# Kernel optimization log

Measured on AMD Instinct MI355X. Metric: run time of the kernel, lower is better.

## Reference

```python
import jax, jax.numpy as jnp
import numpy as np

N_NODES = 100000


def gcn_conv(x, W, b, src, dst, n_nodes):
    """PyG GCNConv: out = D^{-1/2} (A + I) D^{-1/2} X W + b."""
    h = x @ W  # [N, F_out]
    # add self-loops
    loop = jnp.arange(n_nodes, dtype=src.dtype)
    s = jnp.concatenate([src, loop])
    d = jnp.concatenate([dst, loop])
    # symmetric normalization (deg counts incoming edges incl. self-loop)
    deg = jax.ops.segment_sum(jnp.ones_like(d, dtype=h.dtype), d, num_segments=n_nodes)
    dinv = jnp.where(deg > 0, jax.lax.rsqrt(deg), 0.0)
    coef = dinv[s] * dinv[d]  # [E+N]
    msg = h[s] * coef[:, None]  # gather + scale
    out = jax.ops.segment_sum(msg, d, num_segments=n_nodes)  # scatter-add
    return out + b


def setup_inputs() -> dict:
    key = jax.random.key(0)
    k1, k2, k3, k4, k5, k6 = jax.random.split(key, 6)
    in_dim, hidden_dim, out_dim = 128, 64, 64
    n_edges = 1000000
    x = jax.random.normal(k1, (N_NODES, in_dim), dtype=jnp.float32)
    edge_index = jax.random.randint(k2, (2, n_edges), 0, N_NODES, dtype=jnp.int64)
    # glorot-style init for GCN weights
    W1 = jax.random.normal(k3, (in_dim, hidden_dim), dtype=jnp.float32) / np.sqrt(in_dim)
    b1 = jnp.zeros((hidden_dim,), dtype=jnp.float32)
    W2 = jax.random.normal(k4, (hidden_dim, out_dim), dtype=jnp.float32) / np.sqrt(hidden_dim)
    b2 = jnp.zeros((out_dim,), dtype=jnp.float32)
    return {"x": x, "edge_index": edge_index, "W1": W1, "b1": b1, "W2": W2, "b2": b2}


def reference(x, edge_index, W1, b1, W2, b2):
    src, dst = edge_index[0], edge_index[1]
    h = jax.nn.relu(gcn_conv(x, W1, b1, src, dst, N_NODES))
    out = gcn_conv(h, W2, b2, src, dst, N_NODES)
    return out
```

## Files before the change

kernel.cpp:

```cpp
#include <hip/hip_runtime.h>


#define MD 48

typedef __attribute__((ext_vector_type(8))) short bf16x8;
typedef __attribute__((ext_vector_type(4))) float f32x4;
typedef __attribute__((ext_vector_type(2))) float f32x2;
typedef __attribute__((ext_vector_type(4))) int   i32x4;
typedef __attribute__((ext_vector_type(4))) unsigned u32x4;

__device__ inline float bf2f(unsigned short v) {
    unsigned u = (unsigned)v << 16;
    return __builtin_bit_cast(float, u);
}
__device__ inline unsigned short f2bf(float f) {
    unsigned u = __builtin_bit_cast(unsigned, f);
    unsigned r = (u + 0x7FFFu + ((u >> 16) & 1u)) >> 16;
    return (unsigned short)r;
}

__device__ inline void convW_one(const float* __restrict__ W, short* __restrict__ Wth,
                                 short* __restrict__ Wtl, int K, int k, int f) {
    float v = W[k * 64 + f];
    unsigned b = __builtin_bit_cast(unsigned, v);
    unsigned hb = b & 0xFFFF0000u;
    float d = v - __builtin_bit_cast(float, hb);
    unsigned lb = __builtin_bit_cast(unsigned, d);
    Wth[f * K + k] = (short)(hb >> 16);
    Wtl[f * K + k] = (short)(lb >> 16);
}

__global__ __launch_bounds__(256) void k_prep(int* __restrict__ cnt, int n, int nbz,
                                              const float* __restrict__ W1,
                                              short* __restrict__ W1th, short* __restrict__ W1tl,
                                              const float* __restrict__ W2,
                                              short* __restrict__ W2th, short* __restrict__ W2tl) {
    const int b = blockIdx.x;
    if (b < nbz) {
        int i = b * 256 + threadIdx.x;
        if (i < n) cnt[i] = 0;
    } else if (b < nbz + 128) {
        if (threadIdx.x < 64) convW_one(W1, W1th, W1tl, 128, b - nbz, threadIdx.x);
    } else {
        if (threadIdx.x < 64) convW_one(W2, W2th, W2tl, 64, b - nbz - 128, threadIdx.x);
    }
}

__global__ __launch_bounds__(256) void k_fill_xcd(const int* __restrict__ src,
                                                  const int* __restrict__ dst, int E,
                                                  int* __restrict__ cnt,
                                                  int* __restrict__ col_ell,
                                                  int npx, int N) {
    const int myxcd = blockIdx.x & 7;
    const int lo = myxcd * npx;
    const int hi = lo + npx;
    const int vb = blockIdx.x >> 3;
    const int nvb = gridDim.x >> 3;
    const int tid = vb * 256 + threadIdx.x;
    const int nthr = nvb * 256;
    for (int base = tid * 4; base < E; base += nthr * 4) {
        i32x4 d4 = *(const i32x4*)&dst[base];
#pragma unroll
        for (int k = 0; k < 4; ++k) {
            int d = d4[k];
            if (d >= lo && d < hi) {
                int p = atomicAdd(&cnt[d], 1);
                if (p < MD) col_ell[(size_t)p * N + d] = src[base + k];
            }
        }
    }
}

template <int K>
__global__ __launch_bounds__(256) void k_mm_f32A(const float* __restrict__ X,
                                                 const short* __restrict__ Wth,
                                                 const short* __restrict__ Wtl,
                                                 const int* __restrict__ cnt,
                                                 unsigned short* __restrict__ G, int n) {
    const int lane = threadIdx.x & 63;
    const int w = threadIdx.x >> 6;
    const int r0 = lane & 15;
    const int kq = lane >> 4;
    const int arow = blockIdx.x * 64 + w * 16 + r0;
    const float* xrow = X + (size_t)(arow < n ? arow : n - 1) * K;

    f32x4 acc[4] = {};
#pragma unroll
    for (int kc = 0; kc < K / 32; ++kc) {
        const int ks = kc * 32 + kq * 8;
        float xv[8];
        *(f32x4*)&xv[0] = __builtin_nontemporal_load((const f32x4*)&xrow[ks]);
        *(f32x4*)&xv[4] = __builtin_nontemporal_load((const f32x4*)&xrow[ks + 4]);
        bf16x8 ah, al;
#pragma unroll
        for (int j = 0; j < 8; ++j) {
            unsigned b = __builtin_bit_cast(unsigned, xv[j]);
            unsigned hb = b & 0xFFFF0000u;
            float d = xv[j] - __builtin_bit_cast(float, hb);
            unsigned lb = __builtin_bit_cast(unsigned, d);
            ah[j] = (short)(hb >> 16);
            al[j] = (short)(lb >> 16);
        }
#pragma unroll
        for (int c = 0; c < 4; ++c) {
            bf16x8 bh = *(const bf16x8*)&Wth[(c * 16 + r0) * K + ks];
            bf16x8 bl = *(const bf16x8*)&Wtl[(c * 16 + r0) * K + ks];
            acc[c] = __builtin_amdgcn_mfma_f32_16x16x32_bf16(ah, bh, acc[c], 0, 0, 0);
            acc[c] = __builtin_amdgcn_mfma_f32_16x16x32_bf16(ah, bl, acc[c], 0, 0, 0);
            acc[c] = __builtin_amdgcn_mfma_f32_16x16x32_bf16(al, bh, acc[c], 0, 0, 0);
        }
    }
    const int orow = blockIdx.x * 64 + w * 16 + kq * 4;
#pragma unroll
    for (int rg = 0; rg < 4; ++rg) {
        int gr = orow + rg;
        if (gr < n) {
            float di = rsqrtf((float)(cnt[gr] + 1));
#pragma unroll
            for (int c = 0; c < 4; ++c)
                G[(size_t)gr * 64 + c * 16 + r0] = f2bf(acc[c][rg] * di);
        }
    }
}

__global__ __launch_bounds__(256) void k_mm_bf16A(const unsigned short* __restrict__ A,
                                                  const short* __restrict__ Wth,
                                                  const short* __restrict__ Wtl,
                                                  const int* __restrict__ cnt,
                                                  unsigned short* __restrict__ G, int n) {
    constexpr int K = 64;
    const int lane = threadIdx.x & 63;
    const int w = threadIdx.x >> 6;
    const int r0 = lane & 15;
    const int kq = lane >> 4;
    const int arow = blockIdx.x * 64 + w * 16 + r0;
    const unsigned short* ar = A + (size_t)(arow < n ? arow : n - 1) * K;

    f32x4 acc[4] = {};
#pragma unroll
    for (int kc = 0; kc < K / 32; ++kc) {
        const int ks = kc * 32 + kq * 8;
        bf16x8 a = __builtin_nontemporal_load((const bf16x8*)&ar[ks]);
#pragma unroll
        for (int c = 0; c < 4; ++c) {
            bf16x8 bh = *(const bf16x8*)&Wth[(c * 16 + r0) * K + ks];
            bf16x8 bl = *(const bf16x8*)&Wtl[(c * 16 + r0) * K + ks];
            acc[c] = __builtin_amdgcn_mfma_f32_16x16x32_bf16(a, bh, acc[c], 0, 0, 0);
            acc[c] = __builtin_amdgcn_mfma_f32_16x16x32_bf16(a, bl, acc[c], 0, 0, 0);
        }
    }
    const int orow = blockIdx.x * 64 + w * 16 + kq * 4;
#pragma unroll
    for (int rg = 0; rg < 4; ++rg) {
        int gr = orow + rg;
        if (gr < n) {
            float di = rsqrtf((float)(cnt[gr] + 1));
#pragma unroll
            for (int c = 0; c < 4; ++c)
                G[(size_t)gr * 64 + c * 16 + r0] = f2bf(acc[c][rg] * di);
        }
    }
}

template <bool RELU, bool OUTBF>
__global__ __launch_bounds__(256) void k_gather8(const unsigned short* __restrict__ g,
                                                 const int* __restrict__ cntArr,
                                                 const int* __restrict__ col_ell,
                                                 const float* __restrict__ bias,
                                                 void* __restrict__ dest, int n, int N) {
    const int node = blockIdx.x * 4 + (threadIdx.x >> 6);
    if (node >= n) return;
    const int lane = threadIdx.x & 63;
    const int grp = lane >> 3;
    const int fl = lane & 7;
    const int cn = cntArr[node];
    const int lc = min(cn, MD);
    const float dn = rsqrtf((float)(cn + 1));
    const int cl = min(lane, MD - 1);
    const int myidx = col_ell[(size_t)cl * N + node];

    f32x2 acc2[4] = {};
    if (grp == 0) {
        u32x4 u = *(const u32x4*)&g[(size_t)node * 64 + fl * 8];
#pragma unroll
        for (int k = 0; k < 4; ++k) {
            f32x2 f;
            f[0] = __builtin_bit_cast(float, u[k] << 16);
            f[1] = __builtin_bit_cast(float, u[k] & 0xFFFF0000u);
            acc2[k] += f;
        }
    }
    for (int j8 = 0; j8 < lc; j8 += 8) {
        int j = j8 + grp;
        int s = __shfl(myidx, j);
        if (j < lc) {
            u32x4 u = *(const u32x4*)&g[(size_t)s * 64 + fl * 8];
#pragma unroll
            for (int k = 0; k < 4; ++k) {
                f32x2 f;
                f[0] = __builtin_bit_cast(float, u[k] << 16);
                f[1] = __builtin_bit_cast(float, u[k] & 0xFFFF0000u);
                acc2[k] += f;
            }
        }
    }
#pragma unroll
    for (int m = 8; m <= 32; m <<= 1) {
#pragma unroll
        for (int k = 0; k < 4; ++k) {
            f32x2 o;
            o[0] = __shfl_xor(acc2[k][0], m);
            o[1] = __shfl_xor(acc2[k][1], m);
            acc2[k] += o;
        }
    }
    if (grp == 0) {
        float v[8];
        const float* bv = &bias[fl * 8];
#pragma unroll
        for (int k = 0; k < 4; ++k) {
            v[2 * k]     = fmaf(acc2[k][0], dn, bv[2 * k]);
            v[2 * k + 1] = fmaf(acc2[k][1], dn, bv[2 * k + 1]);
            if (RELU) {
                v[2 * k]     = fmaxf(v[2 * k], 0.f);
                v[2 * k + 1] = fmaxf(v[2 * k + 1], 0.f);
            }
        }
        if (OUTBF) {
            u32x4 o;
            o[0] = (unsigned)f2bf(v[0]) | ((unsigned)f2bf(v[1]) << 16);
            o[1] = (unsigned)f2bf(v[2]) | ((unsigned)f2bf(v[3]) << 16);
            o[2] = (unsigned)f2bf(v[4]) | ((unsigned)f2bf(v[5]) << 16);
            o[3] = (unsigned)f2bf(v[6]) | ((unsigned)f2bf(v[7]) << 16);
            *(u32x4*)&((unsigned short*)dest)[(size_t)node * 64 + fl * 8] = o;
        } else {
            float* dp = &((float*)dest)[(size_t)node * 64 + fl * 8];
            __builtin_nontemporal_store(*(const f32x4*)&v[0], (f32x4*)&dp[0]);
            __builtin_nontemporal_store(*(const f32x4*)&v[4], (f32x4*)&dp[4]);
        }
    }
}

extern "C" void kernel_launch(void* const* d_in, const int* in_sizes, int n_in,
                              void* d_out, int out_size, void* d_ws, size_t ws_size,
                              hipStream_t stream) {
    const float* x  = (const float*)d_in[0];
    const int*   ei = (const int*)d_in[1];
    const float* W1 = (const float*)d_in[2];
    const float* b1 = (const float*)d_in[3];
    const float* W2 = (const float*)d_in[4];
    const float* b2 = (const float*)d_in[5];

    const int N = in_sizes[0] / 128;
    const int E = in_sizes[1] / 2;
    const int* src = ei;
    const int* dst = ei + E;
    float* out = (float*)d_out;

    char* ws = (char*)d_ws;
    size_t off = 0;
    auto alloc = [&](size_t bytes) {
        void* p = ws + off;
        off += (bytes + 63) & ~(size_t)63;
        return p;
    };
    unsigned short* a1   = (unsigned short*)alloc((size_t)N * 64 * 2);
    unsigned short* gbuf = (unsigned short*)alloc((size_t)N * 64 * 2);
    int*   cnt     = (int*)alloc((size_t)N * 4);
    int*   col_ell = (int*)alloc((size_t)N * MD * 4);
    short* W1th    = (short*)alloc((size_t)64 * 128 * 2);
    short* W1tl    = (short*)alloc((size_t)64 * 128 * 2);
    short* W2th    = (short*)alloc((size_t)64 * 64 * 2);
    short* W2tl    = (short*)alloc((size_t)64 * 64 * 2);

    const int NBZ   = (N + 255) / 256;
    const int NB_MM = (N + 63) / 64;
    const int NB_G  = (N + 3) / 4;
    const int npx   = (N + 7) / 8;

    k_prep<<<NBZ + 192, 256, 0, stream>>>(cnt, N, NBZ, W1, W1th, W1tl, W2, W2th, W2tl);

    k_fill_xcd<<<8192, 256, 0, stream>>>(src, dst, E, cnt, col_ell, npx, N);

    k_mm_f32A<128><<<NB_MM, 256, 0, stream>>>(x, W1th, W1tl, cnt, gbuf, N);
    k_gather8<true, true><<<NB_G, 256, 0, stream>>>(gbuf, cnt, col_ell, b1, a1, N, N);

    k_mm_bf16A<<<NB_MM, 256, 0, stream>>>(a1, W2th, W2tl, cnt, gbuf, N);
    k_gather8<false, false><<<NB_G, 256, 0, stream>>>(gbuf, cnt, col_ell, b2, out, N, N);
}
```

Before: 203.2 us.

## Switch ELL to row-major layout and gather with two waves per node

The ELL neighbor table changes from column-major (slot-major) to row-major (node-major), so each node's neighbor indices sit contiguously and load in a coalesced way in the gather, though the fill kernel's scattered writes now hit different lines. The gather kernel now splits the 64 features across two waves per node, and each wave has 16 lanes groups handling 16 neighbors per iteration with 4 lanes per 32-feature half. This raises memory-level parallelism per node and halves the loop trip count. The cost is more waves per node and an extra shuffle-reduction stage.

New measurement: 255.1 us. 1.26x slower.

```diff
diff --git a/kernel.cpp b/kernel.cpp
--- a/kernel.cpp
+++ b/kernel.cpp
@@ -49,8 +49,7 @@
 __global__ __launch_bounds__(256) void k_fill_xcd(const int* __restrict__ src,
                                                   const int* __restrict__ dst, int E,
                                                   int* __restrict__ cnt,
-                                                  int* __restrict__ col_ell,
-                                                  int npx, int N) {
+                                                  int* __restrict__ col_ell, int npx) {
     const int myxcd = blockIdx.x & 7;
     const int lo = myxcd * npx;
     const int hi = lo + npx;
@@ -65,7 +64,7 @@
             int d = d4[k];
             if (d >= lo && d < hi) {
                 int p = atomicAdd(&cnt[d], 1);
-                if (p < MD) col_ell[(size_t)p * N + d] = src[base + k];
+                if (p < MD) col_ell[(size_t)d * MD + p] = src[base + k];
             }
         }
     }
@@ -163,38 +162,38 @@
 }
 
 template <bool RELU, bool OUTBF>
-__global__ __launch_bounds__(256) void k_gather8(const unsigned short* __restrict__ g,
-                                                 const int* __restrict__ cntArr,
-                                                 const int* __restrict__ col_ell,
-                                                 const float* __restrict__ bias,
-                                                 void* __restrict__ dest, int n, int N) {
-    const int node = blockIdx.x * 4 + (threadIdx.x >> 6);
+__global__ __launch_bounds__(256) void k_gather16(const unsigned short* __restrict__ g,
+                                                  const int* __restrict__ cntArr,
+                                                  const int* __restrict__ col_ell,
+                                                  const float* __restrict__ bias,
+                                                  void* __restrict__ dest, int n) {
+    const int wid = threadIdx.x >> 6;
+    const int node = blockIdx.x * 2 + (wid >> 1);
     if (node >= n) return;
+    const int whalf = wid & 1;
     const int lane = threadIdx.x & 63;
-    const int grp = lane >> 3;
-    const int fl = lane & 7;
+    const int grp = lane >> 2;
+    const int fq = lane & 3;
+    const int foff = whalf * 32 + fq * 8;
     const int cn = cntArr[node];
     const int lc = min(cn, MD);
     const float dn = rsqrtf((float)(cn + 1));
-    const int cl = min(lane, MD - 1);
-    const int myidx = col_ell[(size_t)cl * N + node];
+    const int myidx = col_ell[(size_t)node * MD + min(lane, MD - 1)];
 
     f32x2 acc2[4] = {};
     if (grp == 0) {
-        u32x4 u = *(const u32x4*)&g[(size_t)node * 64 + fl * 8];
-#pragma unroll
-        for (int k = 0; k < 4; ++k) {
-            f32x2 f;
-            f[0] = __builtin_bit_cast(float, u[k] << 16);
-            f[1] = __builtin_bit_cast(float, u[k] & 0xFFFF0000u);
-            acc2[k] += f;
-        }
-    }
-    for (int j8 = 0; j8 < lc; j8 += 8) {
-        int j = j8 + grp;
+        u32x4 u = *(const u32x4*)&g[(size_t)node * 64 + foff];
+#pragma unroll
+        for (int k = 0; k < 4; ++k) {
+            acc2[k][0] = __builtin_bit_cast(float, u[k] << 16);
+            acc2[k][1] = __builtin_bit_cast(float, u[k] & 0xFFFF0000u);
+        }
+    }
+    for (int j16 = 0; j16 < lc; j16 += 16) {
+        int j = j16 + grp;
         int s = __shfl(myidx, j);
         if (j < lc) {
-            u32x4 u = *(const u32x4*)&g[(size_t)s * 64 + fl * 8];
+            u32x4 u = *(const u32x4*)&g[(size_t)s * 64 + foff];
 #pragma unroll
             for (int k = 0; k < 4; ++k) {
                 f32x2 f;
@@ -205,7 +204,7 @@
         }
     }
 #pragma unroll
-    for (int m = 8; m <= 32; m <<= 1) {
+    for (int m = 4; m <= 32; m <<= 1) {
 #pragma unroll
         for (int k = 0; k < 4; ++k) {
             f32x2 o;
@@ -216,7 +215,7 @@
     }
     if (grp == 0) {
         float v[8];
-        const float* bv = &bias[fl * 8];
+        const float* bv = &bias[foff];
 #pragma unroll
         for (int k = 0; k < 4; ++k) {
             v[2 * k]     = fmaf(acc2[k][0], dn, bv[2 * k]);
@@ -232,9 +231,9 @@
             o[1] = (unsigned)f2bf(v[2]) | ((unsigned)f2bf(v[3]) << 16);
             o[2] = (unsigned)f2bf(v[4]) | ((unsigned)f2bf(v[5]) << 16);
             o[3] = (unsigned)f2bf(v[6]) | ((unsigned)f2bf(v[7]) << 16);
-            *(u32x4*)&((unsigned short*)dest)[(size_t)node * 64 + fl * 8] = o;
+            *(u32x4*)&((unsigned short*)dest)[(size_t)node * 64 + foff] = o;
         } else {
-            float* dp = &((float*)dest)[(size_t)node * 64 + fl * 8];
+            float* dp = &((float*)dest)[(size_t)node * 64 + foff];
             __builtin_nontemporal_store(*(const f32x4*)&v[0], (f32x4*)&dp[0]);
             __builtin_nontemporal_store(*(const f32x4*)&v[4], (f32x4*)&dp[4]);
         }
@@ -267,7 +266,7 @@
     unsigned short* a1   = (unsigned short*)alloc((size_t)N * 64 * 2);
     unsigned short* gbuf = (unsigned short*)alloc((size_t)N * 64 * 2);
     int*   cnt     = (int*)alloc((size_t)N * 4);
-    int*   col_ell = (int*)alloc((size_t)N * MD * 4);
+    int*   col_ell = (int*)alloc(((size_t)N * MD + 64) * 4);
     short* W1th    = (short*)alloc((size_t)64 * 128 * 2);
     short* W1tl    = (short*)alloc((size_t)64 * 128 * 2);
     short* W2th    = (short*)alloc((size_t)64 * 64 * 2);
@@ -275,16 +274,16 @@
 
     const int NBZ   = (N + 255) / 256;
     const int NB_MM = (N + 63) / 64;
-    const int NB_G  = (N + 3) / 4;
+    const int NB_G  = (N + 1) / 2;
     const int npx   = (N + 7) / 8;
 
     k_prep<<<NBZ + 192, 256, 0, stream>>>(cnt, N, NBZ, W1, W1th, W1tl, W2, W2th, W2tl);
 
-    k_fill_xcd<<<8192, 256, 0, stream>>>(src, dst, E, cnt, col_ell, npx, N);
+    k_fill_xcd<<<8192, 256, 0, stream>>>(src, dst, E, cnt, col_ell, npx);
 
     k_mm_f32A<128><<<NB_MM, 256, 0, stream>>>(x, W1th, W1tl, cnt, gbuf, N);
-    k_gather8<true, true><<<NB_G, 256, 0, stream>>>(gbuf, cnt, col_ell, b1, a1, N, N);
+    k_gather16<true, true><<<NB_G, 256, 0, stream>>>(gbuf, cnt, col_ell, b1, a1, N);
 
     k_mm_bf16A<<<NB_MM, 256, 0, stream>>>(a1, W2th, W2tl, cnt, gbuf, N);
-    k_gather8<false, false><<<NB_G, 256, 0, stream>>>(gbuf, cnt, col_ell, b2, out, N, N);
-}
+    k_gather16<false, false><<<NB_G, 256, 0, stream>>>(gbuf, cnt, col_ell, b2, out, N);
+}
```
